# Kernel optimization log

Hardware: AMD Instinct MI355X
Metric: run time of the kernel (lower is better)

The kernel has to match this reference:

```python
import jax, jax.numpy as jnp
import numpy as np

C = 64
CK = C // 8  # query/key channels


def setup_inputs() -> dict:
    key = jax.random.key(0)
    ks = jax.random.split(key, 8)
    b, c, h, w = 4, C, 64, 64
    x = jax.random.normal(ks[0], (b, c, h, w), dtype=jnp.float32)
    # 1x1 conv weights (spectral-normalized weights are still just dense weights at eval)
    wq = jax.random.normal(ks[1], (CK, c), dtype=jnp.float32) * 0.05
    bq = jax.random.normal(ks[2], (CK,), dtype=jnp.float32) * 0.01
    wk = jax.random.normal(ks[3], (CK, c), dtype=jnp.float32) * 0.05
    bk = jax.random.normal(ks[4], (CK,), dtype=jnp.float32) * 0.01
    wv = jax.random.normal(ks[5], (c, c), dtype=jnp.float32) * 0.05
    bv = jax.random.normal(ks[6], (c,), dtype=jnp.float32) * 0.01
    # gamma is initialized to 0 in the module; use a nonzero value so the
    # attention path contributes to the output.
    gamma = jax.random.normal(ks[7], (1,), dtype=jnp.float32) * 0.5
    return {"x": x, "wq": wq, "bq": bq, "wk": wk, "bk": bk,
            "wv": wv, "bv": bv, "gamma": gamma}


def reference(x, wq, bq, wk, bk, wv, bv, gamma):
    b, c, h, w = x.shape
    n = h * w
    xf = x.reshape(b, c, n)                      # [b, c, n]
    # 1x1 convs as matmuls over the channel dim
    q = jnp.einsum('oc,bcn->bno', wq, xf) + bq   # [b, n, ck]
    k = jnp.einsum('oc,bcn->bon', wk, xf) + bk[None, :, None]  # [b, ck, n]
    v = jnp.einsum('oc,bcn->bno', wv, xf) + bv   # [b, n, c]
    attn = jax.nn.softmax(jnp.einsum('bnd,bdm->bnm', q, k), axis=-1)  # [b, n, n]
    o = jnp.einsum('bnm,bmc->bnc', attn, v)      # [b, n, c]
    o = o.transpose(0, 2, 1).reshape(b, c, h, w)
    return gamma[0] * o + x
```

## Files before the change

### kernel.cpp

```cpp
#include <hip/hip_runtime.h>

#define CH 64
#define NN 4096
#define NB 4
#define SPLIT 8
#define KLEN (NN / SPLIT)
#define KTILE 128
#define NT (KLEN / KTILE)
#define QBLK 128
#define LOG2E 1.44269504f

typedef unsigned short u16;
typedef unsigned int u32;
typedef __attribute__((ext_vector_type(8))) short bf16x8;
typedef __attribute__((ext_vector_type(16))) float f32x16;

static __device__ __forceinline__ u16 bf16r(float f) {
  union { float f; unsigned u; } v; v.f = f;
  unsigned x = v.u;
  x += 0x7fffu + ((x >> 16) & 1u);
  return (u16)(x >> 16);
}
static __device__ __forceinline__ u32 pk2(float a, float b) {
  union { float f; unsigned u; } va, vb; va.f = a; vb.f = b;
  unsigned x = va.u, y = vb.u;
  x += 0x7fffu + ((x >> 16) & 1u);
  y += 0x7fffu + ((y >> 16) & 1u);
  return (x >> 16) | (y & 0xffff0000u);
}

__global__ __launch_bounds__(256) void qkv_proj(
    const float* __restrict__ x,
    const float* __restrict__ wq, const float* __restrict__ bq,
    const float* __restrict__ wk, const float* __restrict__ bk,
    const float* __restrict__ wv, const float* __restrict__ bv,
    u16* __restrict__ Qb, u16* __restrict__ Kb, u16* __restrict__ Vb) {
  __shared__ float wvs[64 * 64];
  __shared__ float wqs[8 * 64], wks[8 * 64];
  __shared__ float xs[64 * 64];
  __shared__ float bvs[64], bqs[8], bks[8];
  const int t = threadIdx.x;
  const int blk = blockIdx.x;
  const int b = blk >> 6;
  const int n0 = (blk & 63) << 6;
  const int p = t & 63;
  const int g = t >> 6;
  const float* xb = x + (size_t)b * CH * NN + n0 + p;

  for (int i = t; i < 64 * 64; i += 256) wvs[i] = wv[i];
  for (int i = t; i < 8 * 64; i += 256) { wqs[i] = wq[i]; wks[i] = wk[i]; }
  if (t < 64) bvs[t] = bv[t];
  if (t < 8) { bqs[t] = bq[t]; bks[t] = bk[t]; }
#pragma unroll
  for (int cc = 0; cc < 16; ++cc) {
    const int c = cc * 4 + g;
    xs[c * 64 + p] = xb[(size_t)c * NN];
  }
  __syncthreads();

  const int vch0 = g << 4;
  float vacc[16], aacc[8];
#pragma unroll
  for (int j = 0; j < 16; ++j) vacc[j] = 0.f;
#pragma unroll
  for (int j = 0; j < 8; ++j) aacc[j] = 0.f;
  const float* wA = (g == 0) ? wqs : wks;

  for (int c8 = 0; c8 < 8; ++c8) {
    float xr8[8];
#pragma unroll
    for (int cc = 0; cc < 8; ++cc) xr8[cc] = xs[(c8 * 8 + cc) * 64 + p];
#pragma unroll
    for (int j = 0; j < 16; ++j) {
      const float4 w0 = *reinterpret_cast<const float4*>(&wvs[(vch0 + j) * 64 + c8 * 8]);
      const float4 w1 = *reinterpret_cast<const float4*>(&wvs[(vch0 + j) * 64 + c8 * 8 + 4]);
      vacc[j] = fmaf(w0.x, xr8[0], vacc[j]); vacc[j] = fmaf(w0.y, xr8[1], vacc[j]);
      vacc[j] = fmaf(w0.z, xr8[2], vacc[j]); vacc[j] = fmaf(w0.w, xr8[3], vacc[j]);
      vacc[j] = fmaf(w1.x, xr8[4], vacc[j]); vacc[j] = fmaf(w1.y, xr8[5], vacc[j]);
      vacc[j] = fmaf(w1.z, xr8[6], vacc[j]); vacc[j] = fmaf(w1.w, xr8[7], vacc[j]);
    }
    if (g < 2) {
#pragma unroll
      for (int j = 0; j < 8; ++j) {
        const float4 w0 = *reinterpret_cast<const float4*>(&wA[j * 64 + c8 * 8]);
        const float4 w1 = *reinterpret_cast<const float4*>(&wA[j * 64 + c8 * 8 + 4]);
        aacc[j] = fmaf(w0.x, xr8[0], aacc[j]); aacc[j] = fmaf(w0.y, xr8[1], aacc[j]);
        aacc[j] = fmaf(w0.z, xr8[2], aacc[j]); aacc[j] = fmaf(w0.w, xr8[3], aacc[j]);
        aacc[j] = fmaf(w1.x, xr8[4], aacc[j]); aacc[j] = fmaf(w1.y, xr8[5], aacc[j]);
        aacc[j] = fmaf(w1.z, xr8[6], aacc[j]); aacc[j] = fmaf(w1.w, xr8[7], aacc[j]);
      }
    }
  }

  const int k5 = p & 31;
  const int sperm = (k5 & 19) | ((k5 & 4) << 1) | ((k5 & 8) >> 1);
  const int nstore = n0 + (p & 32) + sperm;
  const size_t vbase = ((size_t)b * CH + vch0) * NN + nstore;
#pragma unroll
  for (int j = 0; j < 16; ++j)
    Vb[vbase + (size_t)j * NN] = bf16r(vacc[j] + bvs[vch0 + j]);

  if (g < 2) {
    const float* bs = (g == 0) ? bqs : bks;
    float o[8];
#pragma unroll
    for (int j = 0; j < 8; ++j) {
      float s = aacc[j] + bs[j];
      o[j] = (g == 0) ? s * LOG2E : s;
    }
    uint4 pkv;
    pkv.x = pk2(o[0], o[1]); pkv.y = pk2(o[2], o[3]);
    pkv.z = pk2(o[4], o[5]); pkv.w = pk2(o[6], o[7]);
    u16* dst = ((g == 0) ? Qb : Kb) + ((size_t)b * NN + n0 + p) * 8;
    *reinterpret_cast<uint4*>(dst) = pkv;
  }
}

__global__ __launch_bounds__(256, 4) void flash_attn(
    const u16* __restrict__ Qb, const u16* __restrict__ Kb,
    const u16* __restrict__ Vb, u32* __restrict__ ACCu,
    float* __restrict__ Lb) {
  __shared__ u16 Klds[2][1032];
  __shared__ u16 Vlds[2][8192];
  const int bid = blockIdx.x;
  const int logical = (bid & 7) * 128 + (bid >> 3);
  const int qb = logical & 31;
  const int b = (logical >> 5) & 3;
  const int sp = logical >> 7;
  const int w = __builtin_amdgcn_readfirstlane(threadIdx.x >> 6);
  const int lane = threadIdx.x & 63;
  const int l31 = lane & 31;
  const int h = lane >> 5;
  const int x7 = l31 & 7;
  const int qrow0 = qb * QBLK + w * 32;
  const int ks = sp * KLEN;

  if (threadIdx.x < 8) {
    Klds[0][1024 + threadIdx.x] = 0;
    Klds[1][1024 + threadIdx.x] = 0;
  }

  bf16x8 qf = {0, 0, 0, 0, 0, 0, 0, 0};
  if (h == 0)
    qf = *reinterpret_cast<const bf16x8*>(Qb + ((size_t)b * NN + qrow0 + l31) * 8);

  const u16* Kp = Kb + ((size_t)b * NN + ks) * 8;
  const u16* Vp = Vb + (size_t)b * CH * NN + ks;

  const int c15 = lane & 15;
  const int r0 = w * 16 + (lane >> 4);
  size_t vsrc[4];
#pragma unroll
  for (int i = 0; i < 4; ++i) {
    const int r = r0 + 4 * i;
    vsrc[i] = (size_t)r * NN + (size_t)(((c15 & 8) | ((c15 ^ r) & 7)) * 8);
  }

#define STAGE(tt, bb) do {                                                    \
    _Pragma("unroll")                                                         \
    for (int i = 0; i < 4; ++i)                                               \
      __builtin_amdgcn_global_load_lds(                                       \
          (const __attribute__((address_space(1))) void*)(Vp + vsrc[i] + (tt) * KTILE), \
          (__attribute__((address_space(3))) void*)&Vlds[bb][(w * 16 + 4 * i) * 128], 16, 0, 0); \
    if (w < 2)                                                                \
      __builtin_amdgcn_global_load_lds(                                       \
          (const __attribute__((address_space(1))) void*)(Kp + ((size_t)(tt) * KTILE + w * 64 + lane) * 8), \
          (__attribute__((address_space(3))) void*)&Klds[bb][w * 512], 16, 0, 0); \
  } while (0)

  f32x16 acc0 = {}, acc1 = {};
  const f32x16 zz = {};
  float lsum = 0.f;

  STAGE(0, 0);
#pragma unroll
  for (int t = 0; t < NT; ++t) {
    const int buf = t & 1;
    __syncthreads();
    if (t + 1 < NT) STAGE(t + 1, buf ^ 1);
    const u16* Kl = &Klds[buf][0];
    const u16* Vl = &Vlds[buf][0];
#pragma unroll
    for (int k32 = 0; k32 < 4; ++k32) {
      const int kaddr = h ? 1024 : (k32 * 32 + l31) * 8;
      bf16x8 kf = *reinterpret_cast<const bf16x8*>(Kl + kaddr);
      f32x16 s = __builtin_amdgcn_mfma_f32_32x32x16_bf16(kf, qf, zz, 0, 0, 0);
      float p[16];
#pragma unroll
      for (int r = 0; r < 16; ++r) { p[r] = exp2f(s[r]); lsum += p[r]; }
      union { uint4 u; bf16x8 v; } pb0, pb1;
      pb0.u.x = pk2(p[0], p[1]);   pb0.u.y = pk2(p[2], p[3]);
      pb0.u.z = pk2(p[4], p[5]);   pb0.u.w = pk2(p[6], p[7]);
      pb1.u.x = pk2(p[8], p[9]);   pb1.u.y = pk2(p[10], p[11]);
      pb1.u.z = pk2(p[12], p[13]); pb1.u.w = pk2(p[14], p[15]);
      const int c16_0 = k32 * 4 + h;
      const int c16_1 = c16_0 + 2;
      const int cp0 = (c16_0 & 8) | ((c16_0 ^ x7) & 7);
      const int cp1 = (c16_1 & 8) | ((c16_1 ^ x7) & 7);
      bf16x8 v00 = *reinterpret_cast<const bf16x8*>(Vl + l31 * 128 + cp0 * 8);
      bf16x8 v01 = *reinterpret_cast<const bf16x8*>(Vl + l31 * 128 + cp1 * 8);
      bf16x8 v10 = *reinterpret_cast<const bf16x8*>(Vl + (32 + l31) * 128 + cp0 * 8);
      bf16x8 v11 = *reinterpret_cast<const bf16x8*>(Vl + (32 + l31) * 128 + cp1 * 8);
      acc0 = __builtin_amdgcn_mfma_f32_32x32x16_bf16(v00, pb0.v, acc0, 0, 0, 0);
      acc0 = __builtin_amdgcn_mfma_f32_32x32x16_bf16(v01, pb1.v, acc0, 0, 0, 0);
      acc1 = __builtin_amdgcn_mfma_f32_32x32x16_bf16(v10, pb0.v, acc1, 0, 0, 0);
      acc1 = __builtin_amdgcn_mfma_f32_32x32x16_bf16(v11, pb1.v, acc1, 0, 0, 0);
    }
  }
#undef STAGE

  lsum += __shfl_xor(lsum, 32);

  const int gtile = b * (NN / 32) + qb * 4 + w;
  u32* A = ACCu + ((size_t)gtile * SPLIT + sp) * 32 * 32;
#pragma unroll
  for (int rp = 0; rp < 8; ++rp) {
    const int chp = (rp & 1) + 4 * (rp >> 1) + 2 * h;
    A[chp * 32 + l31]        = pk2(acc0[2 * rp], acc0[2 * rp + 1]);
    A[(16 + chp) * 32 + l31] = pk2(acc1[2 * rp], acc1[2 * rp + 1]);
  }
  if (h == 0)
    Lb[((size_t)gtile * SPLIT + sp) * 32 + l31] = lsum;
}

__global__ __launch_bounds__(256) void combine(
    const float* __restrict__ x, const float* __restrict__ gamma,
    const u32* __restrict__ ACCu, const float* __restrict__ Lb,
    float* __restrict__ out) {
  const int idx = blockIdx.x * 256 + threadIdx.x;
  const int n4 = idx & (NN / 4 - 1);
  const int cp = (idx >> 10) & 31;
  const int b = idx >> 15;
  const int n = n4 << 2;
  const int gtile = b * (NN / 32) + (n >> 5);
  const int q0 = n & 31;
  const uint4* A4 = reinterpret_cast<const uint4*>(ACCu);
  const float4* L4 = reinterpret_cast<const float4*>(Lb);
  float s0[4] = {0.f, 0.f, 0.f, 0.f}, s1[4] = {0.f, 0.f, 0.f, 0.f};
  float l[4] = {0.f, 0.f, 0.f, 0.f};
#pragma unroll
  for (int sp = 0; sp < SPLIT; ++sp) {
    const uint4 a = A4[(((size_t)gtile * SPLIT + sp) * 32 + cp) * 8 + (q0 >> 2)];
    const float4 lv = L4[(((size_t)gtile * SPLIT + sp) * 32 + q0) >> 2];
    const u32 av[4] = {a.x, a.y, a.z, a.w};
#pragma unroll
    for (int k = 0; k < 4; ++k) {
      union { u32 u; float f; } lo, hi;
      lo.u = av[k] << 16; hi.u = av[k] & 0xffff0000u;
      s0[k] += lo.f; s1[k] += hi.f;
    }
    l[0] += lv.x; l[1] += lv.y; l[2] += lv.z; l[3] += lv.w;
  }
  const float gm = gamma[0];
  float inv[4];
#pragma unroll
  for (int k = 0; k < 4; ++k) inv[k] = gm / l[k];
  const size_t i0 = ((size_t)b * CH + 2 * cp) * NN + n;
  const float4 x0 = *reinterpret_cast<const float4*>(x + i0);
  const float4 x1 = *reinterpret_cast<const float4*>(x + i0 + NN);
  float4 o0, o1;
  o0.x = fmaf(inv[0], s0[0], x0.x); o0.y = fmaf(inv[1], s0[1], x0.y);
  o0.z = fmaf(inv[2], s0[2], x0.z); o0.w = fmaf(inv[3], s0[3], x0.w);
  o1.x = fmaf(inv[0], s1[0], x1.x); o1.y = fmaf(inv[1], s1[1], x1.y);
  o1.z = fmaf(inv[2], s1[2], x1.z); o1.w = fmaf(inv[3], s1[3], x1.w);
  *reinterpret_cast<float4*>(out + i0) = o0;
  *reinterpret_cast<float4*>(out + i0 + NN) = o1;
}

extern "C" void kernel_launch(void* const* d_in, const int* in_sizes, int n_in,
                              void* d_out, int out_size, void* d_ws, size_t ws_size,
                              hipStream_t stream) {
  const float* x     = (const float*)d_in[0];
  const float* wq    = (const float*)d_in[1];
  const float* bq    = (const float*)d_in[2];
  const float* wk    = (const float*)d_in[3];
  const float* bk    = (const float*)d_in[4];
  const float* wv    = (const float*)d_in[5];
  const float* bv    = (const float*)d_in[6];
  const float* gamma = (const float*)d_in[7];
  float* out = (float*)d_out;

  u16* Qb = (u16*)d_ws;
  u16* Kb = Qb + (size_t)NB * NN * 8;
  u16* Vb = Kb + (size_t)NB * NN * 8;
  u32* ACCu = (u32*)(Vb + (size_t)NB * CH * NN);
  float* Lb = (float*)(ACCu + (size_t)NB * (NN / 32) * SPLIT * 32 * 32);

  qkv_proj<<<dim3(NB * (NN / 64)), dim3(256), 0, stream>>>(
      x, wq, bq, wk, bk, wv, bv, Qb, Kb, Vb);
  flash_attn<<<dim3(NB * (NN / QBLK) * SPLIT), dim3(256), 0, stream>>>(
      Qb, Kb, Vb, ACCu, Lb);
  combine<<<dim3((NB * 32 * (NN / 4)) / 256), dim3(256), 0, stream>>>(
      x, gamma, ACCu, Lb, out);
}
```

Baseline: 138.9 us.

## Use MFMA for QKV projection and double query block per attention workgroup

The QKV projection kernel is rewritten to convert weights and inputs to bf16 and compute V, Q and K with 32x32x16 MFMA instructions instead of scalar FMAs in LDS. The flash attention kernel now uses 512-thread blocks covering 256 query rows, so each staged K/V tile is shared by twice as many waves. The block-to-work mapping changes, and partial outputs are written with nontemporal stores. The projection now rounds x to bf16 before the matmul, which adds precision loss, and the larger blocks may lower occupancy.

```diff
diff --git a/kernel.cpp b/kernel.cpp
--- a/kernel.cpp
+++ b/kernel.cpp
@@ -7,7 +7,7 @@
 #define KLEN (NN / SPLIT)
 #define KTILE 128
 #define NT (KLEN / KTILE)
-#define QBLK 128
+#define QBLK 256
 #define LOG2E 1.44269504f
 
 typedef unsigned short u16;
@@ -29,104 +29,100 @@
   return (x >> 16) | (y & 0xffff0000u);
 }
 
-__global__ __launch_bounds__(256) void qkv_proj(
+__global__ __launch_bounds__(128) void qkv_proj(
     const float* __restrict__ x,
     const float* __restrict__ wq, const float* __restrict__ bq,
     const float* __restrict__ wk, const float* __restrict__ bk,
     const float* __restrict__ wv, const float* __restrict__ bv,
     u16* __restrict__ Qb, u16* __restrict__ Kb, u16* __restrict__ Vb) {
-  __shared__ float wvs[64 * 64];
-  __shared__ float wqs[8 * 64], wks[8 * 64];
-  __shared__ float xs[64 * 64];
-  __shared__ float bvs[64], bqs[8], bks[8];
-  const int t = threadIdx.x;
-  const int blk = blockIdx.x;
-  const int b = blk >> 6;
-  const int n0 = (blk & 63) << 6;
-  const int p = t & 63;
-  const int g = t >> 6;
-  const float* xb = x + (size_t)b * CH * NN + n0 + p;
-
-  for (int i = t; i < 64 * 64; i += 256) wvs[i] = wv[i];
-  for (int i = t; i < 8 * 64; i += 256) { wqs[i] = wq[i]; wks[i] = wk[i]; }
-  if (t < 64) bvs[t] = bv[t];
-  if (t < 8) { bqs[t] = bq[t]; bks[t] = bk[t]; }
-#pragma unroll
-  for (int cc = 0; cc < 16; ++cc) {
-    const int c = cc * 4 + g;
-    xs[c * 64 + p] = xb[(size_t)c * NN];
-  }
+  __shared__ u16 afr_lds[3][4][64][8];
+  __shared__ float bvs[64];
+  const int tid = threadIdx.x;
+
+  for (int idx = tid; idx < 3 * 4 * 64; idx += 128) {
+    const int l = idx & 63;
+    const int s = (idx >> 6) & 3;
+    const int t = idx >> 8;
+    const int row = 32 * t + (l & 31);
+    const int c0 = 16 * s + 8 * (l >> 5);
+    float e[8];
+#pragma unroll
+    for (int j = 0; j < 8; ++j) {
+      float v = 0.f;
+      if (row < 64)      v = wv[row * 64 + c0 + j];
+      else if (row < 72) v = wq[(row - 64) * 64 + c0 + j];
+      else if (row < 80) v = wk[(row - 72) * 64 + c0 + j];
+      e[j] = v;
+    }
+    u32* dst = reinterpret_cast<u32*>(&afr_lds[t][s][l][0]);
+    dst[0] = pk2(e[0], e[1]); dst[1] = pk2(e[2], e[3]);
+    dst[2] = pk2(e[4], e[5]); dst[3] = pk2(e[6], e[7]);
+  }
+  if (tid < 64) bvs[tid] = bv[tid];
   __syncthreads();
 
-  const int vch0 = g << 4;
-  float vacc[16], aacc[8];
-#pragma unroll
-  for (int j = 0; j < 16; ++j) vacc[j] = 0.f;
-#pragma unroll
-  for (int j = 0; j < 8; ++j) aacc[j] = 0.f;
-  const float* wA = (g == 0) ? wqs : wks;
-
-  for (int c8 = 0; c8 < 8; ++c8) {
-    float xr8[8];
-#pragma unroll
-    for (int cc = 0; cc < 8; ++cc) xr8[cc] = xs[(c8 * 8 + cc) * 64 + p];
-#pragma unroll
-    for (int j = 0; j < 16; ++j) {
-      const float4 w0 = *reinterpret_cast<const float4*>(&wvs[(vch0 + j) * 64 + c8 * 8]);
-      const float4 w1 = *reinterpret_cast<const float4*>(&wvs[(vch0 + j) * 64 + c8 * 8 + 4]);
-      vacc[j] = fmaf(w0.x, xr8[0], vacc[j]); vacc[j] = fmaf(w0.y, xr8[1], vacc[j]);
-      vacc[j] = fmaf(w0.z, xr8[2], vacc[j]); vacc[j] = fmaf(w0.w, xr8[3], vacc[j]);
-      vacc[j] = fmaf(w1.x, xr8[4], vacc[j]); vacc[j] = fmaf(w1.y, xr8[5], vacc[j]);
-      vacc[j] = fmaf(w1.z, xr8[6], vacc[j]); vacc[j] = fmaf(w1.w, xr8[7], vacc[j]);
-    }
-    if (g < 2) {
-#pragma unroll
-      for (int j = 0; j < 8; ++j) {
-        const float4 w0 = *reinterpret_cast<const float4*>(&wA[j * 64 + c8 * 8]);
-        const float4 w1 = *reinterpret_cast<const float4*>(&wA[j * 64 + c8 * 8 + 4]);
-        aacc[j] = fmaf(w0.x, xr8[0], aacc[j]); aacc[j] = fmaf(w0.y, xr8[1], aacc[j]);
-        aacc[j] = fmaf(w0.z, xr8[2], aacc[j]); aacc[j] = fmaf(w0.w, xr8[3], aacc[j]);
-        aacc[j] = fmaf(w1.x, xr8[4], aacc[j]); aacc[j] = fmaf(w1.y, xr8[5], aacc[j]);
-        aacc[j] = fmaf(w1.z, xr8[6], aacc[j]); aacc[j] = fmaf(w1.w, xr8[7], aacc[j]);
-      }
-    }
-  }
-
-  const int k5 = p & 31;
-  const int sperm = (k5 & 19) | ((k5 & 4) << 1) | ((k5 & 8) >> 1);
-  const int nstore = n0 + (p & 32) + sperm;
-  const size_t vbase = ((size_t)b * CH + vch0) * NN + nstore;
-#pragma unroll
-  for (int j = 0; j < 16; ++j)
-    Vb[vbase + (size_t)j * NN] = bf16r(vacc[j] + bvs[vch0 + j]);
-
-  if (g < 2) {
-    const float* bs = (g == 0) ? bqs : bks;
-    float o[8];
-#pragma unroll
-    for (int j = 0; j < 8; ++j) {
-      float s = aacc[j] + bs[j];
-      o[j] = (g == 0) ? s * LOG2E : s;
-    }
-    uint4 pkv;
-    pkv.x = pk2(o[0], o[1]); pkv.y = pk2(o[2], o[3]);
-    pkv.z = pk2(o[4], o[5]); pkv.w = pk2(o[6], o[7]);
-    u16* dst = ((g == 0) ? Qb : Kb) + ((size_t)b * NN + n0 + p) * 8;
-    *reinterpret_cast<uint4*>(dst) = pkv;
-  }
-}
-
-__global__ __launch_bounds__(256, 4) void flash_attn(
+  const int b = blockIdx.x >> 6;
+  const int n0 = (blockIdx.x & 63) << 6;
+  const int w = tid >> 6;
+  const int lane = tid & 63;
+  const int l31 = lane & 31;
+  const int h = lane >> 5;
+  const int n = n0 + 32 * w + l31;
+
+  bf16x8 afr[3][4];
+#pragma unroll
+  for (int t = 0; t < 3; ++t)
+#pragma unroll
+    for (int s = 0; s < 4; ++s)
+      afr[t][s] = *reinterpret_cast<const bf16x8*>(&afr_lds[t][s][lane][0]);
+
+  f32x16 acc[3] = {{}, {}, {}};
+  const float* xb = x + (size_t)b * CH * NN + n;
+#pragma unroll
+  for (int s = 0; s < 4; ++s) {
+    float xv[8];
+#pragma unroll
+    for (int j = 0; j < 8; ++j)
+      xv[j] = xb[(size_t)(16 * s + 8 * h + j) * NN];
+    union { uint4 u; bf16x8 v; } bf;
+    bf.u.x = pk2(xv[0], xv[1]); bf.u.y = pk2(xv[2], xv[3]);
+    bf.u.z = pk2(xv[4], xv[5]); bf.u.w = pk2(xv[6], xv[7]);
+#pragma unroll
+    for (int t = 0; t < 3; ++t)
+      acc[t] = __builtin_amdgcn_mfma_f32_32x32x16_bf16(afr[t][s], bf.v, acc[t], 0, 0, 0);
+  }
+
+  const int sperm = (l31 & 19) | ((l31 & 4) << 1) | ((l31 & 8) >> 1);
+  const int nperm = n0 + 32 * w + sperm;
+#pragma unroll
+  for (int t = 0; t < 2; ++t)
+#pragma unroll
+    for (int r = 0; r < 16; ++r) {
+      const int row = 32 * t + (r & 3) + 8 * (r >> 2) + 4 * h;
+      Vb[((size_t)b * CH + row) * NN + nperm] = bf16r(acc[t][r] + bvs[row]);
+    }
+#pragma unroll
+  for (int r = 0; r < 8; ++r) {
+    const int row = (r & 3) + 8 * (r >> 2) + 4 * h;
+    const float v = acc[2][r];
+    if (row < 8)
+      Qb[((size_t)b * NN + n) * 8 + row] = bf16r((v + bq[row]) * LOG2E);
+    else
+      Kb[((size_t)b * NN + n) * 8 + (row - 8)] = bf16r(v + bk[row - 8]);
+  }
+}
+
+__global__ __launch_bounds__(512, 4) void flash_attn(
     const u16* __restrict__ Qb, const u16* __restrict__ Kb,
     const u16* __restrict__ Vb, u32* __restrict__ ACCu,
     float* __restrict__ Lb) {
   __shared__ u16 Klds[2][1032];
   __shared__ u16 Vlds[2][8192];
   const int bid = blockIdx.x;
-  const int logical = (bid & 7) * 128 + (bid >> 3);
-  const int qb = logical & 31;
-  const int b = (logical >> 5) & 3;
-  const int sp = logical >> 7;
+  const int sp = bid & 7;
+  const int rest = bid >> 3;
+  const int qb = rest & 15;
+  const int b = rest >> 4;
   const int w = __builtin_amdgcn_readfirstlane(threadIdx.x >> 6);
   const int lane = threadIdx.x & 63;
   const int l31 = lane & 31;
@@ -148,20 +144,18 @@
   const u16* Vp = Vb + (size_t)b * CH * NN + ks;
 
   const int c15 = lane & 15;
-  const int r0 = w * 16 + (lane >> 4);
-  size_t vsrc[4];
-#pragma unroll
-  for (int i = 0; i < 4; ++i) {
-    const int r = r0 + 4 * i;
-    vsrc[i] = (size_t)r * NN + (size_t)(((c15 & 8) | ((c15 ^ r) & 7)) * 8);
-  }
+  const int vr0 = w * 8 + (lane >> 4);
+  const int vr1 = vr0 + 4;
+  const size_t vsrc0 = (size_t)vr0 * NN + (size_t)(((c15 & 8) | ((c15 ^ vr0) & 7)) * 8);
+  const size_t vsrc1 = (size_t)vr1 * NN + (size_t)(((c15 & 8) | ((c15 ^ vr1) & 7)) * 8);
 
 #define STAGE(tt, bb) do {                                                    \
-    _Pragma("unroll")                                                         \
-    for (int i = 0; i < 4; ++i)                                               \
-      __builtin_amdgcn_global_load_lds(                                       \
-          (const __attribute__((address_space(1))) void*)(Vp + vsrc[i] + (tt) * KTILE), \
-          (__attribute__((address_space(3))) void*)&Vlds[bb][(w * 16 + 4 * i) * 128], 16, 0, 0); \
+    __builtin_amdgcn_global_load_lds(                                         \
+        (const __attribute__((address_space(1))) void*)(Vp + vsrc0 + (tt) * KTILE), \
+        (__attribute__((address_space(3))) void*)&Vlds[bb][(w * 8) * 128], 16, 0, 0); \
+    __builtin_amdgcn_global_load_lds(                                         \
+        (const __attribute__((address_space(1))) void*)(Vp + vsrc1 + (tt) * KTILE), \
+        (__attribute__((address_space(3))) void*)&Vlds[bb][(w * 8 + 4) * 128], 16, 0, 0); \
     if (w < 2)                                                                \
       __builtin_amdgcn_global_load_lds(                                       \
           (const __attribute__((address_space(1))) void*)(Kp + ((size_t)(tt) * KTILE + w * 64 + lane) * 8), \
@@ -211,16 +205,18 @@
 
   lsum += __shfl_xor(lsum, 32);
 
-  const int gtile = b * (NN / 32) + qb * 4 + w;
+  const int gtile = b * (NN / 32) + qb * 8 + w;
   u32* A = ACCu + ((size_t)gtile * SPLIT + sp) * 32 * 32;
 #pragma unroll
   for (int rp = 0; rp < 8; ++rp) {
     const int chp = (rp & 1) + 4 * (rp >> 1) + 2 * h;
-    A[chp * 32 + l31]        = pk2(acc0[2 * rp], acc0[2 * rp + 1]);
-    A[(16 + chp) * 32 + l31] = pk2(acc1[2 * rp], acc1[2 * rp + 1]);
+    __builtin_nontemporal_store(pk2(acc0[2 * rp], acc0[2 * rp + 1]),
+                                &A[chp * 32 + l31]);
+    __builtin_nontemporal_store(pk2(acc1[2 * rp], acc1[2 * rp + 1]),
+                                &A[(16 + chp) * 32 + l31]);
   }
   if (h == 0)
-    Lb[((size_t)gtile * SPLIT + sp) * 32 + l31] = lsum;
+    __builtin_nontemporal_store(lsum, &Lb[((size_t)gtile * SPLIT + sp) * 32 + l31]);
 }
 
 __global__ __launch_bounds__(256) void combine(
@@ -286,9 +282,9 @@
   u32* ACCu = (u32*)(Vb + (size_t)NB * CH * NN);
   float* Lb = (float*)(ACCu + (size_t)NB * (NN / 32) * SPLIT * 32 * 32);
 
-  qkv_proj<<<dim3(NB * (NN / 64)), dim3(256), 0, stream>>>(
+  qkv_proj<<<dim3(NB * (NN / 64)), dim3(128), 0, stream>>>(
       x, wq, bq, wk, bk, wv, bv, Qb, Kb, Vb);
-  flash_attn<<<dim3(NB * (NN / QBLK) * SPLIT), dim3(256), 0, stream>>>(
+  flash_attn<<<dim3(NB * (NN / QBLK) * SPLIT), dim3(512), 0, stream>>>(
       Qb, Kb, Vb, ACCu, Lb);
   combine<<<dim3((NB * 32 * (NN / 4)) / 256), dim3(256), 0, stream>>>(
       x, gamma, ACCu, Lb, out);
```

New measurement: 134.5 us. -3.2%, faster.
